# Optimization experiments

Measured on AMD Instinct MI355X. Metric: run time of the kernel, lower is better.

The kernel has to match this reference:

```python
import jax, jax.numpy as jnp
import numpy as np

N_HEADS = 4
ATT_DIM = 640  # 10 * n_channels
SCALE = ATT_DIM ** (-0.5)


def setup_inputs() -> dict:
    key = jax.random.key(0)
    k1, k2, k3, k4, k5 = jax.random.split(key, 5)
    C, HpA = 64, N_HEADS * ATT_DIM  # 64, 2560
    x = jax.random.normal(k1, (8, C, 32, 32), dtype=jnp.float32)
    W_proj = jax.random.normal(k2, (C, 3 * HpA), dtype=jnp.float32) * (C ** -0.5)
    b_proj = jax.random.normal(k3, (3 * HpA,), dtype=jnp.float32) * 0.02
    W_out = jax.random.normal(k4, (HpA, C), dtype=jnp.float32) * (HpA ** -0.5)
    b_out = jax.random.normal(k5, (C,), dtype=jnp.float32) * 0.02
    return {"x": x, "t": 0, "W_proj": W_proj, "b_proj": b_proj, "W_out": W_out, "b_out": b_out}


def reference(x, t, W_proj, b_proj, W_out, b_out):
    del t  # unused, matches original signature
    b, c, w, h = x.shape
    seq = w * h
    xs = x.reshape(b, c, seq).transpose(0, 2, 1)  # [b, seq, C]
    proj = (xs @ W_proj + b_proj).reshape(b, seq, N_HEADS, 3 * ATT_DIM)
    q, k, v = jnp.split(proj, 3, axis=-1)  # each [b, seq, H, D]
    # scores [b, i, j, h]; NOTE softmax over axis=1 (queries), non-standard
    prod = jnp.einsum('bihd,bjhd->bijh', q, k) * SCALE
    soft = jax.nn.softmax(prod, axis=1)
    att = jnp.einsum('bijh,bjhd->bihd', soft, v)  # [b, seq, H, D]
    out = att.reshape(b, seq, N_HEADS * ATT_DIM) @ W_out + b_out  # [b, seq, C]
    out = out + xs
    return out.reshape(b, w, h, c).transpose(0, 3, 1, 2)
```

## Files before the change

kernel.cpp:

```cpp
#include <hip/hip_runtime.h>
#include <hip/hip_bf16.h>
#include <stdint.h>

typedef unsigned short u16;
typedef __attribute__((ext_vector_type(4))) float f32x4;
typedef __attribute__((ext_vector_type(8))) short bf16x8;

#define DEV __device__ __forceinline__

DEV float bf2f(u16 b){ unsigned u = ((unsigned)b) << 16; return __builtin_bit_cast(float, u); }
DEV u16 f2bf(float f){
  unsigned u = __builtin_bit_cast(unsigned, f);
  u += 0x7FFFu + ((u >> 16) & 1u);
  return (u16)(u >> 16);
}

DEV int xcd_swz(int nwg){
  const int bid = (int)blockIdx.x;
  return (bid & 7) * (nwg >> 3) + (bid >> 3);
}

DEV void stage_x64(const u16* srcbase, u16* dst, int tid){
  #pragma unroll
  for (int q = 0; q < 4; q++) {
    const int boff = q * 4096 + tid * 16;
    const int row = boff >> 7, slot = (boff & 127) >> 4;
    const int kk = (slot ^ (row & 7)) << 3;
    __builtin_amdgcn_global_load_lds(
        (const __attribute__((address_space(1))) void*)(srcbase + (long)row * 64 + kk),
        (__attribute__((address_space(3))) void*)(dst + (boff >> 1)), 16, 0, 0);
  }
}

DEV void tr_tile(float (*tile)[65], const float* src, u16* dst,
                 int R, int C, int r0, int c0)
{
  const int t = threadIdx.x;
  const int rr = t >> 2, cc = (t & 3) * 16;
  const float* sp = src + (long)(r0 + rr) * C + (c0 + cc);
  #pragma unroll
  for (int q = 0; q < 16; q++) tile[rr][cc + q] = sp[q];
  __syncthreads();
  u16* dp = dst + (long)(c0 + rr) * R + (r0 + cc);
  #pragma unroll
  for (int q = 0; q < 16; q++) dp[q] = f2bf(tile[cc + q][rr]);
}

__global__ __launch_bounds__(256) void k_misc(
    const float* __restrict__ x, const float* __restrict__ Wp,
    const float* __restrict__ Wo, const float* __restrict__ bp,
    u16* __restrict__ xt, u16* __restrict__ Wot, u16* __restrict__ Wpb,
    u16* __restrict__ xb, float* __restrict__ uh)
{
  __shared__ float tile[64][65];
  const int q = blockIdx.x;
  if (q < 240) {
    const long i = (long)q * 256 + threadIdx.x;
    const f32x4 a = *(const f32x4*)(Wp + i * 8);
    const f32x4 b = *(const f32x4*)(Wp + i * 8 + 4);
    bf16x8 r;
    #pragma unroll
    for (int e = 0; e < 4; e++){ r[e] = (short)f2bf(a[e]); r[e+4] = (short)f2bf(b[e]); }
    *(bf16x8*)(Wpb + i * 8) = r;
  } else if (q < 368) {
    const int p = q - 240, c0 = (p & 15) * 64, b = p >> 4;
    tr_tile(tile, x + (long)b * 65536, xt + (long)b * 65536, 64, 1024, 0, c0);
  } else if (q < 408) {
    const int p = q - 368;
    tr_tile(tile, Wo, Wot, 2560, 64, p * 64, 0);
  } else if (q < 472) {
    const int p = q - 408;
    const int wv = threadIdx.x >> 6, lane = threadIdx.x & 63;
    const int idx = p * 4 + wv;
    const int h = idx >> 6, c = idx & 63;
    const int qb = h * 1920, kb = qb + 640;
    const float* wrow = Wp + (long)c * 7680 + qb;
    float s = 0.f;
    #pragma unroll
    for (int d0 = 0; d0 < 640; d0 += 64)
      s += wrow[d0 + lane] * bp[kb + d0 + lane];
    #pragma unroll
    for (int off = 32; off; off >>= 1) s += __shfl_down(s, off);
    if (lane == 0) uh[idx] = s;
  } else {
    const int ch = (q - 472) * 256 + threadIdx.x;
    const int b = ch / 10240, rem = ch % 10240;
    const int row = rem >> 7, j8 = rem & 127;
    bf16x8 r;
    if (row < 64) {
      const float* sp = x + ((long)b * 64 + row) * 1024 + j8 * 8;
      const f32x4 a = *(const f32x4*)sp;
      const f32x4 bb = *(const f32x4*)(sp + 4);
      #pragma unroll
      for (int e = 0; e < 4; e++){ r[e] = (short)f2bf(a[e]); r[e+4] = (short)f2bf(bb[e]); }
    } else if (row == 64) {
      #pragma unroll
      for (int e = 0; e < 8; e++) r[e] = (short)0x3F80;
    } else {
      #pragma unroll
      for (int e = 0; e < 8; e++) r[e] = 0;
    }
    *(bf16x8*)(xb + ((long)b * 80 + row) * 1024 + j8 * 8) = r;
  }
}

__global__ __launch_bounds__(256) void k_nh(
    const u16* __restrict__ Wot, const float* __restrict__ bp,
    u16* __restrict__ MxT)
{
  const int wv = threadIdx.x >> 6, lane = threadIdx.x & 63;
  const int idx = blockIdx.x * 4 + wv;
  const int h = idx >> 6, cp = idx & 63;
  const u16* wr_ = Wot + (long)cp * 2560 + h * 640;
  const float* bv = bp + h * 1920 + 1280;
  float s = 0.f;
  #pragma unroll
  for (int d0 = 0; d0 < 640; d0 += 64)
    s += bf2f(wr_[d0 + lane]) * bv[d0 + lane];
  #pragma unroll
  for (int off = 32; off; off >>= 1) s += __shfl_down(s, off);
  if (lane == 0) MxT[cp * 320 + h * 80 + 64] = f2bf(s);
  if (lane >= 1 && lane < 16) MxT[cp * 320 + h * 80 + 64 + lane] = 0;
}

template<int BM, int BN, int BK, int WR, int WC, int MF, int NF>
DEV void gemm_nt(const u16* __restrict__ A, const u16* __restrict__ B,
                 int K, long lda, long ldb, int arow0, int brow0,
                 f32x4 (&acc)[MF][NF], u16* As, u16* Bs)
{
  const int tid  = threadIdx.x;
  const int lane = tid & 63;
  const int w    = tid >> 6;
  const int wr   = w / WC, wc = w % WC;
  constexpr int NT   = WR * WC * 64;
  constexpr int AISS = (BM * BK * 2) / (NT * 16);
  constexpr int BISS = (BN * BK * 2) / (NT * 16);
  constexpr int ABUF = BM * BK;
  constexpr int BBUF = BN * BK;

  #pragma unroll
  for (int m = 0; m < MF; m++)
    #pragma unroll
    for (int n = 0; n < NF; n++) acc[m][n] = f32x4{0.f, 0.f, 0.f, 0.f};

  const int frow = lane & 15;
  const int fs   = lane >> 4;

  auto stage = [&](int buf, int kt) {
    #pragma unroll
    for (int q = 0; q < AISS; q++) {
      const int boff = q * NT * 16 + tid * 16;
      const int row  = boff / (BK * 2);
      const int slot = (boff % (BK * 2)) >> 4;
      const int kk   = ((slot ^ (row & 7)) << 3);
      const u16* src = A + (long)(arow0 + row) * lda + kt + kk;
      __builtin_amdgcn_global_load_lds(
          (const __attribute__((address_space(1))) void*)src,
          (__attribute__((address_space(3))) void*)(As + buf * ABUF + (boff >> 1)), 16, 0, 0);
    }
    #pragma unroll
    for (int q = 0; q < BISS; q++) {
      const int boff = q * NT * 16 + tid * 16;
      const int row  = boff / (BK * 2);
      const int slot = (boff % (BK * 2)) >> 4;
      const int kk   = ((slot ^ (row & 7)) << 3);
      const u16* src = B + (long)(brow0 + row) * ldb + kt + kk;
      __builtin_amdgcn_global_load_lds(
          (const __attribute__((address_space(1))) void*)src,
          (__attribute__((address_space(3))) void*)(Bs + buf * BBUF + (boff >> 1)), 16, 0, 0);
    }
  };

  auto compute = [&](int buf) {
    __builtin_amdgcn_s_setprio(1);
    #pragma unroll
    for (int ks = 0; ks < BK / 32; ++ks) {
      bf16x8 af[MF], bfr[NF];
      #pragma unroll
      for (int m = 0; m < MF; m++) {
        const int row  = wr * (MF * 16) + m * 16 + frow;
        const int slot = (ks * 4 + fs) ^ (row & 7);
        af[m] = *(const bf16x8*)(As + buf * ABUF + row * BK + slot * 8);
      }
      #pragma unroll
      for (int n = 0; n < NF; n++) {
        const int row  = wc * (NF * 16) + n * 16 + frow;
        const int slot = (ks * 4 + fs) ^ (row & 7);
        bfr[n] = *(const bf16x8*)(Bs + buf * BBUF + row * BK + slot * 8);
      }
      #pragma unroll
      for (int m = 0; m < MF; m++)
        #pragma unroll
        for (int n = 0; n < NF; n++)
          acc[m][n] = __builtin_amdgcn_mfma_f32_16x16x32_bf16(af[m], bfr[n], acc[m][n], 0, 0, 0);
    }
    __builtin_amdgcn_s_setprio(0);
  };

  stage(0, 0);
  asm volatile("s_waitcnt vmcnt(0)" ::: "memory");
  __syncthreads();
  int cur = 0;
  for (int kt = BK; kt < K; kt += BK) {
    stage(cur ^ 1, kt);
    compute(cur);
    asm volatile("s_waitcnt vmcnt(0)" ::: "memory");
    __syncthreads();
    cur ^= 1;
  }
  compute(cur);
}

template<int MF, int NF, typename FV, typename FS>
DEV void epi_u16(u16* SH, FV&& fval, FS&& fstore)
{
  constexpr int RC = MF * 16, CC = NF * 16, CPR = NF * 2;
  const int lane = threadIdx.x & 63;
  const int w = threadIdx.x >> 6;
  u16* et = SH + w * (RC * CC);
  __syncthreads();
  #pragma unroll
  for (int m = 0; m < MF; m++)
    #pragma unroll
    for (int n = 0; n < NF; n++)
      #pragma unroll
      for (int j = 0; j < 4; j++) {
        const int row = m * 16 + (lane >> 4) * 4 + j;
        const int col = n * 16 + (lane & 15);
        et[row * CC + (((col >> 3) ^ row) & (CPR - 1)) * 8 + (col & 7)] =
            f2bf(fval(m, n, j, row, col));
      }
  constexpr int RPI = 64 / CPR;
  #pragma unroll
  for (int it = 0; it < RC / RPI; ++it) {
    const int row = it * RPI + lane / CPR;
    const int ch  = lane % CPR;
    bf16x8 v = *(const bf16x8*)(et + row * CC + ((ch ^ row) & (CPR - 1)) * 8);
    fstore(row, ch * 8, v);
  }
}

__global__ __launch_bounds__(256) void k_prep(
    const u16* __restrict__ Wpb, const u16* __restrict__ Wot,
    u16* __restrict__ Ahat, u16* __restrict__ MxT)
{
  __shared__ __align__(16) u16 SH[4 * 64 * 64];
  u16* As = SH; u16* Bs = SH + 2 * 64 * 64;
  const int q = blockIdx.x;
  const int w = threadIdx.x >> 6;
  const int wr = w >> 1, wc = w & 1;
  f32x4 acc[2][2];
  if (q < 4) {
    const int h = q;
    gemm_nt<64, 64, 64, 2, 2, 2, 2>(Wpb + h * 1920 + 640, Wpb + h * 1920, 640,
                                    7680, 7680, 0, 0, acc, As, Bs);
    u16* dst = Ahat + h * 4096;
    epi_u16<2, 2>(SH,
      [&](int m, int n, int j, int row, int col){ return acc[m][n][j]; },
      [&](int row, int c0, bf16x8 v){
        *(bf16x8*)(dst + (wr * 32 + row) * 64 + wc * 32 + c0) = v; });
  } else {
    const int h = q - 4;
    gemm_nt<64, 64, 64, 2, 2, 2, 2>(Wot + h * 640, Wpb + h * 1920 + 1280, 640,
                                    2560, 7680, 0, 0, acc, As, Bs);
    epi_u16<2, 2>(SH,
      [&](int m, int n, int j, int row, int col){ return acc[m][n][j]; },
      [&](int row, int c0, bf16x8 v){
        *(bf16x8*)(MxT + (long)(wr * 32 + row) * 320 + h * 80 + wc * 32 + c0) = v; });
  }
}

__global__ __launch_bounds__(256) void k_qkz(
    const u16* __restrict__ xt, const u16* __restrict__ Ahat,
    const float* __restrict__ uh, float* __restrict__ Z)
{
  __shared__ __align__(16) u16 XI[2][8192];
  __shared__ __align__(16) u16 AH[4096];
  __shared__ __align__(16) u16 XJ[8192];
  __shared__ __align__(16) u16 TT[8192];
  __shared__ float uts[128];
  __shared__ float uhl[64];
  __shared__ float Zs[2][128];
  const int tid = threadIdx.x, lane = tid & 63, w = tid >> 6;
  const int frow = lane & 15, fs = lane >> 4;
  const int wr = w >> 1, wc = w & 1;
  const int id = xcd_swz(256);
  const int bh = id >> 3, tj = id & 7;
  const int b = bh >> 2, h = bh & 3;
  const int j0 = b * 1024 + tj * 128;

  #pragma unroll
  for (int q = 0; q < 2; q++) {
    const int boff = q * 4096 + tid * 16;
    const int row = boff >> 7, slot = (boff & 127) >> 4;
    const int kk = (slot ^ (row & 7)) << 3;
    __builtin_amdgcn_global_load_lds(
        (const __attribute__((address_space(1))) void*)(Ahat + h * 4096 + row * 64 + kk),
        (__attribute__((address_space(3))) void*)(AH + (boff >> 1)), 16, 0, 0);
  }
  stage_x64(xt + (long)j0 * 64, XJ, tid);
  stage_x64(xt + (long)(b * 1024) * 64, XI[0], tid);
  if (tid < 64) uhl[tid] = uh[h * 64 + tid];
  asm volatile("s_waitcnt vmcnt(0)" ::: "memory");
  __syncthreads();

  float csum[4] = {0.f, 0.f, 0.f, 0.f};
  int cur = 0;
  for (int it = 0; it < 8; ++it) {
    if (it < 7) stage_x64(xt + (long)(b * 1024 + (it + 1) * 128) * 64, XI[cur ^ 1], tid);
    f32x4 acc1[4][2];
    #pragma unroll
    for (int m = 0; m < 4; m++)
      #pragma unroll
      for (int n = 0; n < 2; n++) acc1[m][n] = f32x4{0.f, 0.f, 0.f, 0.f};
    #pragma unroll
    for (int ks = 0; ks < 2; ks++) {
      bf16x8 af[4], bfr[2];
      #pragma unroll
      for (int m = 0; m < 4; m++) {
        const int row = wr * 64 + m * 16 + frow;
        af[m] = *(const bf16x8*)(XI[cur] + row * 64 + (((ks * 4 + fs) ^ (row & 7)) << 3));
      }
      #pragma unroll
      for (int n = 0; n < 2; n++) {
        const int row = wc * 32 + n * 16 + frow;
        bfr[n] = *(const bf16x8*)(AH + row * 64 + (((ks * 4 + fs) ^ (row & 7)) << 3));
      }
      #pragma unroll
      for (int m = 0; m < 4; m++)
        #pragma unroll
        for (int n = 0; n < 2; n++)
          acc1[m][n] = __builtin_amdgcn_mfma_f32_16x16x32_bf16(af[m], bfr[n], acc1[m][n], 0, 0, 0);
    }
    float su = 0.f;
    if (tid < 128) {
      #pragma unroll
      for (int s = 0; s < 8; s++) {
        bf16x8 v = *(const bf16x8*)(XI[cur] + tid * 64 + ((s ^ (tid & 7)) << 3));
        #pragma unroll
        for (int e = 0; e < 8; e++) su += bf2f((u16)v[e]) * uhl[s * 8 + e];
      }
    }
    __syncthreads();
    if (tid < 128) uts[tid] = su;
    #pragma unroll
    for (int m = 0; m < 4; m++)
      #pragma unroll
      for (int n = 0; n < 2; n++)
        #pragma unroll
        for (int j = 0; j < 4; j++) {
          const int row = wr * 64 + m * 16 + (lane >> 4) * 4 + j;
          const int col = wc * 32 + n * 16 + (lane & 15);
          TT[row * 64 + (((col >> 3) ^ (row & 7)) << 3) + (col & 7)] = f2bf(acc1[m][n][j]);
        }
    asm volatile("s_waitcnt vmcnt(0)" ::: "memory");
    __syncthreads();
    f32x4 sacc[4][4];
    #pragma unroll
    for (int m = 0; m < 4; m++)
      #pragma unroll
      for (int n = 0; n < 4; n++) sacc[m][n] = f32x4{0.f, 0.f, 0.f, 0.f};
    #pragma unroll
    for (int ks = 0; ks < 2; ks++) {
      bf16x8 af[4], bfr[4];
      #pragma unroll
      for (int m = 0; m < 4; m++) {
        const int row = wr * 64 + m * 16 + frow;
        af[m] = *(const bf16x8*)(TT + row * 64 + (((ks * 4 + fs) ^ (row & 7)) << 3));
      }
      #pragma unroll
      for (int n = 0; n < 4; n++) {
        const int row = wc * 64 + n * 16 + frow;
        bfr[n] = *(const bf16x8*)(XJ + row * 64 + (((ks * 4 + fs) ^ (row & 7)) << 3));
      }
      #pragma unroll
      for (int m = 0; m < 4; m++)
        #pragma unroll
        for (int n = 0; n < 4; n++)
          sacc[m][n] = __builtin_amdgcn_mfma_f32_16x16x32_bf16(af[m], bfr[n], sacc[m][n], 0, 0, 0);
    }
    #pragma unroll
    for (int m = 0; m < 4; m++)
      #pragma unroll
      for (int j = 0; j < 4; j++) {
        const float rv = uts[wr * 64 + m * 16 + (lane >> 4) * 4 + j];
        #pragma unroll
        for (int n = 0; n < 4; n++)
          csum[n] += __expf((sacc[m][n][j] + rv) * 0.03952847075210474f);
      }
    cur ^= 1;
  }
  #pragma unroll
  for (int n = 0; n < 4; n++) {
    csum[n] += __shfl_xor(csum[n], 16);
    csum[n] += __shfl_xor(csum[n], 32);
  }
  if ((lane >> 4) == 0) {
    #pragma unroll
    for (int n = 0; n < 4; n++) Zs[wr][wc * 64 + n * 16 + lane] = csum[n];
  }
  __syncthreads();
  if (tid < 128) Z[(long)bh * 1024 + tj * 128 + tid] = Zs[0][tid] + Zs[1][tid];
}

__global__ __launch_bounds__(256) void k_G(
    const u16* __restrict__ xt, const u16* __restrict__ xb,
    const u16* __restrict__ Ahat, const float* __restrict__ uh,
    const float* __restrict__ Z, u16* __restrict__ G)
{
  __shared__ __align__(16) u16 XIT[8192];
  __shared__ __align__(16) u16 AH[4096];
  __shared__ __align__(16) u16 XJ[2][8192];
  __shared__ __align__(16) u16 XB[10240];
  __shared__ __align__(16) u16 PT[16384];
  __shared__ float uts[128];
  __shared__ float uhl[64];
  __shared__ float rzs[128];
  const int tid = threadIdx.x, lane = tid & 63, w = tid >> 6;
  const int frow = lane & 15, fs = lane >> 4;
  const int wr = w >> 1, wc = w & 1;
  const int id = xcd_swz(256);
  const int bh = id >> 3, ti = id & 7;
  const int b = bh >> 2, h = bh & 3;
  const int i0 = b * 1024 + ti * 128;

  #pragma unroll
  for (int q = 0; q < 2; q++) {
    const int boff = q * 4096 + tid * 16;
    const int row = boff >> 7, slot = (boff & 127) >> 4;
    const int kk = (slot ^ (row & 7)) << 3;
    __builtin_amdgcn_global_load_lds(
        (const __attribute__((address_space(1))) void*)(Ahat + h * 4096 + row * 64 + kk),
        (__attribute__((address_space(3))) void*)(AH + (boff >> 1)), 16, 0, 0);
  }
  stage_x64(xt + (long)i0 * 64, XIT, tid);
  stage_x64(xt + (long)(b * 1024) * 64, XJ[0], tid);
  if (tid < 64) uhl[tid] = uh[h * 64 + tid];
  asm volatile("s_waitcnt vmcnt(0)" ::: "memory");
  __syncthreads();

  f32x4 acc1[4][2];
  #pragma unroll
  for (int m = 0; m < 4; m++)
    #pragma unroll
    for (int n = 0; n < 2; n++) acc1[m][n] = f32x4{0.f, 0.f, 0.f, 0.f};
  #pragma unroll
  for (int ks = 0; ks < 2; ks++) {
    bf16x8 af[4], bfr[2];
    #pragma unroll
    for (int m = 0; m < 4; m++) {
      const int row = wr * 64 + m * 16 + frow;
      af[m] = *(const bf16x8*)(XIT + row * 64 + (((ks * 4 + fs) ^ (row & 7)) << 3));
    }
    #pragma unroll
    for (int n = 0; n < 2; n++) {
      const int row = wc * 32 + n * 16 + frow;
      bfr[n] = *(const bf16x8*)(AH + row * 64 + (((ks * 4 + fs) ^ (row & 7)) << 3));
    }
    #pragma unroll
    for (int m = 0; m < 4; m++)
      #pragma unroll
      for (int n = 0; n < 2; n++)
        acc1[m][n] = __builtin_amdgcn_mfma_f32_16x16x32_bf16(af[m], bfr[n], acc1[m][n], 0, 0, 0);
  }
  float su = 0.f;
  if (tid < 128) {
    #pragma unroll
    for (int s = 0; s < 8; s++) {
      bf16x8 v = *(const bf16x8*)(XIT + tid * 64 + ((s ^ (tid & 7)) << 3));
      #pragma unroll
      for (int e = 0; e < 8; e++) su += bf2f((u16)v[e]) * uhl[s * 8 + e];
    }
  }
  __syncthreads();
  if (tid < 128) uts[tid] = su;
  #pragma unroll
  for (int m = 0; m < 4; m++)
    #pragma unroll
    for (int n = 0; n < 2; n++)
      #pragma unroll
      for (int j = 0; j < 4; j++) {
        const int row = wr * 64 + m * 16 + (lane >> 4) * 4 + j;
        const int col = wc * 32 + n * 16 + (lane & 15);
        XIT[row * 64 + (((col >> 3) ^ (row & 7)) << 3) + (col & 7)] = f2bf(acc1[m][n][j]);
      }
  __syncthreads();

  f32x4 gacc[2][5];
  #pragma unroll
  for (int m = 0; m < 2; m++)
    #pragma unroll
    for (int n = 0; n < 5; n++) gacc[m][n] = f32x4{0.f, 0.f, 0.f, 0.f};
  int cur = 0;
  for (int j = 0; j < 8; ++j) {
    #pragma unroll
    for (int q = 0; q < 5; q++) {
      const int boff = q * 4096 + tid * 16;
      const int c = boff >> 8, sl = (boff & 255) >> 4;
      const int kk = (sl ^ (c & 7)) << 3;
      __builtin_amdgcn_global_load_lds(
          (const __attribute__((address_space(1))) void*)(xb + ((long)b * 80 + c) * 1024 + j * 128 + kk),
          (__attribute__((address_space(3))) void*)(XB + (boff >> 1)), 16, 0, 0);
    }
    if (j < 7) stage_x64(xt + (long)(b * 1024 + (j + 1) * 128) * 64, XJ[cur ^ 1], tid);
    if (tid < 128) rzs[tid] = 1.0f / Z[(long)bh * 1024 + j * 128 + tid];
    f32x4 sacc[4][4];
    #pragma unroll
    for (int m = 0; m < 4; m++)
      #pragma unroll
      for (int n = 0; n < 4; n++) sacc[m][n] = f32x4{0.f, 0.f, 0.f, 0.f};
    #pragma unroll
    for (int ks = 0; ks < 2; ks++) {
      bf16x8 af[4], bfr[4];
      #pragma unroll
      for (int m = 0; m < 4; m++) {
        const int row = wr * 64 + m * 16 + frow;
        af[m] = *(const bf16x8*)(XIT + row * 64 + (((ks * 4 + fs) ^ (row & 7)) << 3));
      }
      #pragma unroll
      for (int n = 0; n < 4; n++) {
        const int row = wc * 64 + n * 16 + frow;
        bfr[n] = *(const bf16x8*)(XJ[cur] + row * 64 + (((ks * 4 + fs) ^ (row & 7)) << 3));
      }
      #pragma unroll
      for (int m = 0; m < 4; m++)
        #pragma unroll
        for (int n = 0; n < 4; n++)
          sacc[m][n] = __builtin_amdgcn_mfma_f32_16x16x32_bf16(af[m], bfr[n], sacc[m][n], 0, 0, 0);
    }
    __syncthreads();
    #pragma unroll
    for (int m = 0; m < 4; m++)
      #pragma unroll
      for (int jj = 0; jj < 4; jj++) {
        const int row = wr * 64 + m * 16 + (lane >> 4) * 4 + jj;
        const float rv = uts[row];
        #pragma unroll
        for (int n = 0; n < 4; n++) {
          const int col = wc * 64 + n * 16 + (lane & 15);
          const float p = __expf((sacc[m][n][jj] + rv) * 0.03952847075210474f) * rzs[col];
          PT[row * 128 + (((col >> 3) ^ (row & 7)) << 3) + (col & 7)] = f2bf(p);
        }
      }
    asm volatile("s_waitcnt vmcnt(0)" ::: "memory");
    __syncthreads();
    #pragma unroll
    for (int ks = 0; ks < 4; ks++) {
      bf16x8 af2[2], bfr2[5];
      #pragma unroll
      for (int m = 0; m < 2; m++) {
        const int row = w * 32 + m * 16 + frow;
        af2[m] = *(const bf16x8*)(PT + row * 128 + (((ks * 4 + fs) ^ (row & 7)) << 3));
      }
      #pragma unroll
      for (int n = 0; n < 5; n++) {
        const int rc = n * 16 + frow;
        bfr2[n] = *(const bf16x8*)(XB + rc * 128 + (((ks * 4 + fs) ^ (rc & 7)) << 3));
      }
      #pragma unroll
      for (int m = 0; m < 2; m++)
        #pragma unroll
        for (int n = 0; n < 5; n++)
          gacc[m][n] = __builtin_amdgcn_mfma_f32_16x16x32_bf16(af2[m], bfr2[n], gacc[m][n], 0, 0, 0);
    }
    __syncthreads();
    cur ^= 1;
  }
  #pragma unroll
  for (int m = 0; m < 2; m++)
    #pragma unroll
    for (int n = 0; n < 5; n++)
      #pragma unroll
      for (int jj = 0; jj < 4; jj++) {
        const int row = w * 32 + m * 16 + (lane >> 4) * 4 + jj;
        const int col = n * 16 + (lane & 15);
        PT[row * 80 + col] = f2bf(gacc[m][n][jj]);
      }
  __syncthreads();
  #pragma unroll
  for (int it = 0; it < 5; ++it) {
    const int task = it * 256 + tid;
    const int row = task / 10, ch = task % 10;
    bf16x8 v = *(const bf16x8*)(PT + row * 80 + ch * 8);
    *(bf16x8*)(G + (long)(i0 + row) * 320 + h * 80 + ch * 8) = v;
  }
}

__global__ __launch_bounds__(256) void k_out(
    const u16* __restrict__ G, const u16* __restrict__ MxT,
    const float* __restrict__ bo, const float* __restrict__ x, float* __restrict__ out)
{
  __shared__ __align__(16) u16 SH[2 * 128 * 64 + 2 * 64 * 64];
  u16* As = SH; u16* Bs = SH + 2 * 128 * 64;
  f32x4 acc[2][4];
  gemm_nt<128, 64, 64, 4, 1, 2, 4>(G, MxT, 320, 320, 320,
                                   blockIdx.x * 128, 0, acc, As, Bs);
  const int lane = threadIdx.x & 63;
  const int wr = threadIdx.x >> 6;
  float* etf = (float*)SH;
  __syncthreads();
  #pragma unroll
  for (int m = 0; m < 2; m++)
    #pragma unroll
    for (int n = 0; n < 4; n++)
      #pragma unroll
      for (int j = 0; j < 4; j++) {
        const int sl = wr * 32 + m * 16 + (lane >> 4) * 4 + j;
        const int c  = n * 16 + (lane & 15);
        etf[c * 132 + sl] = acc[m][n][j];
      }
  __syncthreads();
  const int b = blockIdx.x >> 3, s0 = (blockIdx.x & 7) * 128;
  #pragma unroll
  for (int it = 0; it < 8; ++it) {
    const int task = it * 256 + threadIdx.x;
    const int c = task >> 5, q = (task & 31) * 4;
    const float bias = bo[c];
    f32x4 v = *(const f32x4*)(etf + c * 132 + q);
    const long xi = ((long)(b * 64 + c) << 10) + s0 + q;
    const f32x4 xv = *(const f32x4*)(x + xi);
    #pragma unroll
    for (int e = 0; e < 4; e++) v[e] += bias + xv[e];
    *(f32x4*)(out + xi) = v;
  }
}

extern "C" void kernel_launch(void* const* d_in, const int* in_sizes, int n_in,
                              void* d_out, int out_size, void* d_ws, size_t ws_size,
                              hipStream_t stream)
{
  (void)in_sizes; (void)n_in; (void)out_size; (void)ws_size;
  const float* x  = (const float*)d_in[0];
  const float* Wp = (const float*)d_in[2];
  const float* bp = (const float*)d_in[3];
  const float* Wo = (const float*)d_in[4];
  const float* bo = (const float*)d_in[5];
  float* out = (float*)d_out;

  char* w8 = (char*)d_ws;
  u16*   xt   = (u16*)(w8 + 0L);
  u16*   xb   = (u16*)(w8 + 1048576L);
  u16*   Wot  = (u16*)(w8 + 2359296L);
  u16*   Wpb  = (u16*)(w8 + 2686976L);
  u16*   Ahat = (u16*)(w8 + 3670016L);
  u16*   MxT  = (u16*)(w8 + 3702784L);
  float* uh   = (float*)(w8 + 3743744L);
  float* Z    = (float*)(w8 + 3744768L);
  u16*   G    = (u16*)(w8 + 3875840L);

  k_misc<<<792, 256, 0, stream>>>(x, Wp, Wo, bp, xt, Wot, Wpb, xb, uh);
  k_nh  <<<64,  256, 0, stream>>>(Wot, bp, MxT);
  k_prep<<<8,   256, 0, stream>>>(Wpb, Wot, Ahat, MxT);
  k_qkz <<<256, 256, 0, stream>>>(xt, Ahat, uh, Z);
  k_G   <<<256, 256, 0, stream>>>(xt, xb, Ahat, uh, Z, G);
  k_out <<<64,  256, 0, stream>>>(G, MxT, bo, x, out);
}
```

Baseline: 76.74 us.

## Split Z reduction across i-halves, widen k_G to 512 threads, fold k_nh into k_misc

k_qkz now launches 512 blocks, each covering half of the query tiles and writing a partial column sum. k_G sums the two partials when it computes the reciprocal. k_G moves to 512 threads (8 waves) with smaller per-wave tiles, which raises wave-level parallelism per CU and lowers register pressure. The separate k_nh launch is folded into an extra k_misc block that reads fp32 Wo directly, removing one kernel launch, though that single block does serial 640-step loops.

```diff
diff --git a/kernel.cpp b/kernel.cpp
--- a/kernel.cpp
+++ b/kernel.cpp
@@ -20,15 +20,20 @@
   return (bid & 7) * (nwg >> 3) + (bid >> 3);
 }
 
+DEV void gld16(const u16* src, u16* dst){
+  __builtin_amdgcn_global_load_lds(
+      (const __attribute__((address_space(1))) void*)src,
+      (__attribute__((address_space(3))) void*)dst, 16, 0, 0);
+}
+
+template<int NTH>
 DEV void stage_x64(const u16* srcbase, u16* dst, int tid){
   #pragma unroll
-  for (int q = 0; q < 4; q++) {
-    const int boff = q * 4096 + tid * 16;
+  for (int q = 0; q < 16384 / (NTH * 16); q++) {
+    const int boff = q * NTH * 16 + tid * 16;
     const int row = boff >> 7, slot = (boff & 127) >> 4;
     const int kk = (slot ^ (row & 7)) << 3;
-    __builtin_amdgcn_global_load_lds(
-        (const __attribute__((address_space(1))) void*)(srcbase + (long)row * 64 + kk),
-        (__attribute__((address_space(3))) void*)(dst + (boff >> 1)), 16, 0, 0);
+    gld16(srcbase + (long)row * 64 + kk, dst + (boff >> 1));
   }
 }
 
@@ -50,7 +55,7 @@
     const float* __restrict__ x, const float* __restrict__ Wp,
     const float* __restrict__ Wo, const float* __restrict__ bp,
     u16* __restrict__ xt, u16* __restrict__ Wot, u16* __restrict__ Wpb,
-    u16* __restrict__ xb, float* __restrict__ uh)
+    u16* __restrict__ xb, float* __restrict__ uh, u16* __restrict__ MxT)
 {
   __shared__ float tile[64][65];
   const int q = blockIdx.x;
@@ -82,7 +87,7 @@
     #pragma unroll
     for (int off = 32; off; off >>= 1) s += __shfl_down(s, off);
     if (lane == 0) uh[idx] = s;
-  } else {
+  } else if (q < 792) {
     const int ch = (q - 472) * 256 + threadIdx.x;
     const int b = ch / 10240, rem = ch % 10240;
     const int row = rem >> 7, j8 = rem & 127;
@@ -101,26 +106,17 @@
       for (int e = 0; e < 8; e++) r[e] = 0;
     }
     *(bf16x8*)(xb + ((long)b * 80 + row) * 1024 + j8 * 8) = r;
-  }
-}
-
-__global__ __launch_bounds__(256) void k_nh(
-    const u16* __restrict__ Wot, const float* __restrict__ bp,
-    u16* __restrict__ MxT)
-{
-  const int wv = threadIdx.x >> 6, lane = threadIdx.x & 63;
-  const int idx = blockIdx.x * 4 + wv;
-  const int h = idx >> 6, cp = idx & 63;
-  const u16* wr_ = Wot + (long)cp * 2560 + h * 640;
-  const float* bv = bp + h * 1920 + 1280;
-  float s = 0.f;
-  #pragma unroll
-  for (int d0 = 0; d0 < 640; d0 += 64)
-    s += bf2f(wr_[d0 + lane]) * bv[d0 + lane];
-  #pragma unroll
-  for (int off = 32; off; off >>= 1) s += __shfl_down(s, off);
-  if (lane == 0) MxT[cp * 320 + h * 80 + 64] = f2bf(s);
-  if (lane >= 1 && lane < 16) MxT[cp * 320 + h * 80 + 64 + lane] = 0;
+  } else {
+    const int wv = threadIdx.x >> 6, lane = threadIdx.x & 63;
+    const float* bv = bp + wv * 1920 + 1280;
+    float s = 0.f;
+    #pragma unroll 8
+    for (int d = 0; d < 640; d++)
+      s += Wo[(long)(wv * 640 + d) * 64 + lane] * bv[d];
+    MxT[lane * 320 + wv * 80 + 64] = f2bf(s);
+    #pragma unroll
+    for (int e = 1; e < 16; e++) MxT[lane * 320 + wv * 80 + 64 + e] = 0;
+  }
 }
 
 template<int BM, int BN, int BK, int WR, int WC, int MF, int NF>
@@ -153,10 +149,7 @@
       const int row  = boff / (BK * 2);
       const int slot = (boff % (BK * 2)) >> 4;
       const int kk   = ((slot ^ (row & 7)) << 3);
-      const u16* src = A + (long)(arow0 + row) * lda + kt + kk;
-      __builtin_amdgcn_global_load_lds(
-          (const __attribute__((address_space(1))) void*)src,
-          (__attribute__((address_space(3))) void*)(As + buf * ABUF + (boff >> 1)), 16, 0, 0);
+      gld16(A + (long)(arow0 + row) * lda + kt + kk, As + buf * ABUF + (boff >> 1));
     }
     #pragma unroll
     for (int q = 0; q < BISS; q++) {
@@ -164,10 +157,7 @@
       const int row  = boff / (BK * 2);
       const int slot = (boff % (BK * 2)) >> 4;
       const int kk   = ((slot ^ (row & 7)) << 3);
-      const u16* src = B + (long)(brow0 + row) * ldb + kt + kk;
-      __builtin_amdgcn_global_load_lds(
-          (const __attribute__((address_space(1))) void*)src,
-          (__attribute__((address_space(3))) void*)(Bs + buf * BBUF + (boff >> 1)), 16, 0, 0);
+      gld16(B + (long)(brow0 + row) * ldb + kt + kk, Bs + buf * BBUF + (boff >> 1));
     }
   };
 
@@ -272,7 +262,7 @@
 
 __global__ __launch_bounds__(256) void k_qkz(
     const u16* __restrict__ xt, const u16* __restrict__ Ahat,
-    const float* __restrict__ uh, float* __restrict__ Z)
+    const float* __restrict__ uh, float* __restrict__ Zp)
 {
   __shared__ __align__(16) u16 XI[2][8192];
   __shared__ __align__(16) u16 AH[4096];
@@ -284,30 +274,30 @@
   const int tid = threadIdx.x, lane = tid & 63, w = tid >> 6;
   const int frow = lane & 15, fs = lane >> 4;
   const int wr = w >> 1, wc = w & 1;
-  const int id = xcd_swz(256);
-  const int bh = id >> 3, tj = id & 7;
+  const int id = xcd_swz(512);
+  const int bh = id >> 4, rem = id & 15;
+  const int tj = rem >> 1, ihalf = rem & 1;
   const int b = bh >> 2, h = bh & 3;
   const int j0 = b * 1024 + tj * 128;
+  const int itb = ihalf * 4;
 
   #pragma unroll
   for (int q = 0; q < 2; q++) {
     const int boff = q * 4096 + tid * 16;
     const int row = boff >> 7, slot = (boff & 127) >> 4;
     const int kk = (slot ^ (row & 7)) << 3;
-    __builtin_amdgcn_global_load_lds(
-        (const __attribute__((address_space(1))) void*)(Ahat + h * 4096 + row * 64 + kk),
-        (__attribute__((address_space(3))) void*)(AH + (boff >> 1)), 16, 0, 0);
-  }
-  stage_x64(xt + (long)j0 * 64, XJ, tid);
-  stage_x64(xt + (long)(b * 1024) * 64, XI[0], tid);
+    gld16(Ahat + h * 4096 + row * 64 + kk, AH + (boff >> 1));
+  }
+  stage_x64<256>(xt + (long)j0 * 64, XJ, tid);
+  stage_x64<256>(xt + (long)(b * 1024 + itb * 128) * 64, XI[0], tid);
   if (tid < 64) uhl[tid] = uh[h * 64 + tid];
   asm volatile("s_waitcnt vmcnt(0)" ::: "memory");
   __syncthreads();
 
   float csum[4] = {0.f, 0.f, 0.f, 0.f};
   int cur = 0;
-  for (int it = 0; it < 8; ++it) {
-    if (it < 7) stage_x64(xt + (long)(b * 1024 + (it + 1) * 128) * 64, XI[cur ^ 1], tid);
+  for (int it = 0; it < 4; ++it) {
+    if (it < 3) stage_x64<256>(xt + (long)(b * 1024 + (itb + it + 1) * 128) * 64, XI[cur ^ 1], tid);
     f32x4 acc1[4][2];
     #pragma unroll
     for (int m = 0; m < 4; m++)
@@ -400,13 +390,14 @@
     for (int n = 0; n < 4; n++) Zs[wr][wc * 64 + n * 16 + lane] = csum[n];
   }
   __syncthreads();
-  if (tid < 128) Z[(long)bh * 1024 + tj * 128 + tid] = Zs[0][tid] + Zs[1][tid];
-}
-
-__global__ __launch_bounds__(256) void k_G(
+  if (tid < 128)
+    Zp[(long)(ihalf * 32 + bh) * 1024 + tj * 128 + tid] = Zs[0][tid] + Zs[1][tid];
+}
+
+__global__ __launch_bounds__(512) void k_G(
     const u16* __restrict__ xt, const u16* __restrict__ xb,
     const u16* __restrict__ Ahat, const float* __restrict__ uh,
-    const float* __restrict__ Z, u16* __restrict__ G)
+    const float* __restrict__ Zp, u16* __restrict__ G)
 {
   __shared__ __align__(16) u16 XIT[8192];
   __shared__ __align__(16) u16 AH[4096];
@@ -418,50 +409,40 @@
   __shared__ float rzs[128];
   const int tid = threadIdx.x, lane = tid & 63, w = tid >> 6;
   const int frow = lane & 15, fs = lane >> 4;
-  const int wr = w >> 1, wc = w & 1;
+  const int twr = w >> 2, twc = w & 3;
   const int id = xcd_swz(256);
   const int bh = id >> 3, ti = id & 7;
   const int b = bh >> 2, h = bh & 3;
   const int i0 = b * 1024 + ti * 128;
 
-  #pragma unroll
-  for (int q = 0; q < 2; q++) {
-    const int boff = q * 4096 + tid * 16;
+  {
+    const int boff = tid * 16;
     const int row = boff >> 7, slot = (boff & 127) >> 4;
     const int kk = (slot ^ (row & 7)) << 3;
-    __builtin_amdgcn_global_load_lds(
-        (const __attribute__((address_space(1))) void*)(Ahat + h * 4096 + row * 64 + kk),
-        (__attribute__((address_space(3))) void*)(AH + (boff >> 1)), 16, 0, 0);
-  }
-  stage_x64(xt + (long)i0 * 64, XIT, tid);
-  stage_x64(xt + (long)(b * 1024) * 64, XJ[0], tid);
+    gld16(Ahat + h * 4096 + row * 64 + kk, AH + (boff >> 1));
+  }
+  stage_x64<512>(xt + (long)i0 * 64, XIT, tid);
+  stage_x64<512>(xt + (long)(b * 1024) * 64, XJ[0], tid);
   if (tid < 64) uhl[tid] = uh[h * 64 + tid];
   asm volatile("s_waitcnt vmcnt(0)" ::: "memory");
   __syncthreads();
 
-  f32x4 acc1[4][2];
-  #pragma unroll
-  for (int m = 0; m < 4; m++)
-    #pragma unroll
-    for (int n = 0; n < 2; n++) acc1[m][n] = f32x4{0.f, 0.f, 0.f, 0.f};
+  f32x4 acc1[4];
+  #pragma unroll
+  for (int m = 0; m < 4; m++) acc1[m] = f32x4{0.f, 0.f, 0.f, 0.f};
   #pragma unroll
   for (int ks = 0; ks < 2; ks++) {
-    bf16x8 af[4], bfr[2];
+    bf16x8 af[4], bfr;
     #pragma unroll
     for (int m = 0; m < 4; m++) {
-      const int row = wr * 64 + m * 16 + frow;
+      const int row = twr * 64 + m * 16 + frow;
       af[m] = *(const bf16x8*)(XIT + row * 64 + (((ks * 4 + fs) ^ (row & 7)) << 3));
     }
-    #pragma unroll
-    for (int n = 0; n < 2; n++) {
-      const int row = wc * 32 + n * 16 + frow;
-      bfr[n] = *(const bf16x8*)(AH + row * 64 + (((ks * 4 + fs) ^ (row & 7)) << 3));
-    }
+    const int rowb = twc * 16 + frow;
+    bfr = *(const bf16x8*)(AH + rowb * 64 + (((ks * 4 + fs) ^ (rowb & 7)) << 3));
     #pragma unroll
     for (int m = 0; m < 4; m++)
-      #pragma unroll
-      for (int n = 0; n < 2; n++)
-        acc1[m][n] = __builtin_amdgcn_mfma_f32_16x16x32_bf16(af[m], bfr[n], acc1[m][n], 0, 0, 0);
+      acc1[m] = __builtin_amdgcn_mfma_f32_16x16x32_bf16(af[m], bfr, acc1[m], 0, 0, 0);
   }
   float su = 0.f;
   if (tid < 128) {
@@ -477,55 +458,57 @@
   #pragma unroll
   for (int m = 0; m < 4; m++)
     #pragma unroll
-    for (int n = 0; n < 2; n++)
-      #pragma unroll
-      for (int j = 0; j < 4; j++) {
-        const int row = wr * 64 + m * 16 + (lane >> 4) * 4 + j;
-        const int col = wc * 32 + n * 16 + (lane & 15);
-        XIT[row * 64 + (((col >> 3) ^ (row & 7)) << 3) + (col & 7)] = f2bf(acc1[m][n][j]);
-      }
-  __syncthreads();
-
-  f32x4 gacc[2][5];
-  #pragma unroll
-  for (int m = 0; m < 2; m++)
-    #pragma unroll
-    for (int n = 0; n < 5; n++) gacc[m][n] = f32x4{0.f, 0.f, 0.f, 0.f};
+    for (int j = 0; j < 4; j++) {
+      const int row = twr * 64 + m * 16 + (lane >> 4) * 4 + j;
+      const int col = twc * 16 + (lane & 15);
+      XIT[row * 64 + (((col >> 3) ^ (row & 7)) << 3) + (col & 7)] = f2bf(acc1[m][j]);
+    }
+  __syncthreads();
+
+  f32x4 gacc[5];
+  #pragma unroll
+  for (int n = 0; n < 5; n++) gacc[n] = f32x4{0.f, 0.f, 0.f, 0.f};
   int cur = 0;
   for (int j = 0; j < 8; ++j) {
     #pragma unroll
-    for (int q = 0; q < 5; q++) {
-      const int boff = q * 4096 + tid * 16;
+    for (int q = 0; q < 2; q++) {
+      const int boff = q * 8192 + tid * 16;
       const int c = boff >> 8, sl = (boff & 255) >> 4;
       const int kk = (sl ^ (c & 7)) << 3;
-      __builtin_amdgcn_global_load_lds(
-          (const __attribute__((address_space(1))) void*)(xb + ((long)b * 80 + c) * 1024 + j * 128 + kk),
-          (__attribute__((address_space(3))) void*)(XB + (boff >> 1)), 16, 0, 0);
-    }
-    if (j < 7) stage_x64(xt + (long)(b * 1024 + (j + 1) * 128) * 64, XJ[cur ^ 1], tid);
-    if (tid < 128) rzs[tid] = 1.0f / Z[(long)bh * 1024 + j * 128 + tid];
-    f32x4 sacc[4][4];
+      gld16(xb + ((long)b * 80 + c) * 1024 + j * 128 + kk, XB + (boff >> 1));
+    }
+    if (tid < 256) {
+      const int boff = 16384 + tid * 16;
+      const int c = boff >> 8, sl = (boff & 255) >> 4;
+      const int kk = (sl ^ (c & 7)) << 3;
+      gld16(xb + ((long)b * 80 + c) * 1024 + j * 128 + kk, XB + (boff >> 1));
+    }
+    if (j < 7) stage_x64<512>(xt + (long)(b * 1024 + (j + 1) * 128) * 64, XJ[cur ^ 1], tid);
+    if (tid < 128)
+      rzs[tid] = 1.0f / (Zp[(long)bh * 1024 + j * 128 + tid] +
+                         Zp[(long)(32 + bh) * 1024 + j * 128 + tid]);
+    f32x4 sacc[4][2];
     #pragma unroll
     for (int m = 0; m < 4; m++)
       #pragma unroll
-      for (int n = 0; n < 4; n++) sacc[m][n] = f32x4{0.f, 0.f, 0.f, 0.f};
+      for (int n = 0; n < 2; n++) sacc[m][n] = f32x4{0.f, 0.f, 0.f, 0.f};
     #pragma unroll
     for (int ks = 0; ks < 2; ks++) {
-      bf16x8 af[4], bfr[4];
+      bf16x8 af[4], bfr[2];
       #pragma unroll
       for (int m = 0; m < 4; m++) {
-        const int row = wr * 64 + m * 16 + frow;
+        const int row = twr * 64 + m * 16 + frow;
         af[m] = *(const bf16x8*)(XIT + row * 64 + (((ks * 4 + fs) ^ (row & 7)) << 3));
       }
       #pragma unroll
-      for (int n = 0; n < 4; n++) {
-        const int row = wc * 64 + n * 16 + frow;
+      for (int n = 0; n < 2; n++) {
+        const int row = twc * 32 + n * 16 + frow;
         bfr[n] = *(const bf16x8*)(XJ[cur] + row * 64 + (((ks * 4 + fs) ^ (row & 7)) << 3));
       }
       #pragma unroll
       for (int m = 0; m < 4; m++)
         #pragma unroll
-        for (int n = 0; n < 4; n++)
+        for (int n = 0; n < 2; n++)
           sacc[m][n] = __builtin_amdgcn_mfma_f32_16x16x32_bf16(af[m], bfr[n], sacc[m][n], 0, 0, 0);
     }
     __syncthreads();
@@ -533,11 +516,11 @@
     for (int m = 0; m < 4; m++)
       #pragma unroll
       for (int jj = 0; jj < 4; jj++) {
-        const int row = wr * 64 + m * 16 + (lane >> 4) * 4 + jj;
+        const int row = twr * 64 + m * 16 + (lane >> 4) * 4 + jj;
         const float rv = uts[row];
         #pragma unroll
-        for (int n = 0; n < 4; n++) {
-          const int col = wc * 64 + n * 16 + (lane & 15);
+        for (int n = 0; n < 2; n++) {
+          const int col = twc * 32 + n * 16 + (lane & 15);
           const float p = __expf((sacc[m][n][jj] + rv) * 0.03952847075210474f) * rzs[col];
           PT[row * 128 + (((col >> 3) ^ (row & 7)) << 3) + (col & 7)] = f2bf(p);
         }
@@ -546,40 +529,39 @@
     __syncthreads();
     #pragma unroll
     for (int ks = 0; ks < 4; ks++) {
-      bf16x8 af2[2], bfr2[5];
-      #pragma unroll
-      for (int m = 0; m < 2; m++) {
-        const int row = w * 32 + m * 16 + frow;
-        af2[m] = *(const bf16x8*)(PT + row * 128 + (((ks * 4 + fs) ^ (row & 7)) << 3));
-      }
+      bf16x8 af2, bfr2[5];
+      const int row = w * 16 + frow;
+      af2 = *(const bf16x8*)(PT + row * 128 + (((ks * 4 + fs) ^ (row & 7)) << 3));
       #pragma unroll
       for (int n = 0; n < 5; n++) {
         const int rc = n * 16 + frow;
         bfr2[n] = *(const bf16x8*)(XB + rc * 128 + (((ks * 4 + fs) ^ (rc & 7)) << 3));
       }
       #pragma unroll
-      for (int m = 0; m < 2; m++)
-        #pragma unroll
-        for (int n = 0; n < 5; n++)
-          gacc[m][n] = __builtin_amdgcn_mfma_f32_16x16x32_bf16(af2[m], bfr2[n], gacc[m][n], 0, 0, 0);
+      for (int n = 0; n < 5; n++)
+        gacc[n] = __builtin_amdgcn_mfma_f32_16x16x32_bf16(af2, bfr2[n], gacc[n], 0, 0, 0);
     }
     __syncthreads();
     cur ^= 1;
   }
   #pragma unroll
-  for (int m = 0; m < 2; m++)
-    #pragma unroll
-    for (int n = 0; n < 5; n++)
-      #pragma unroll
-      for (int jj = 0; jj < 4; jj++) {
-        const int row = w * 32 + m * 16 + (lane >> 4) * 4 + jj;
-        const int col = n * 16 + (lane & 15);
-        PT[row * 80 + col] = f2bf(gacc[m][n][jj]);
-      }
-  __syncthreads();
-  #pragma unroll
-  for (int it = 0; it < 5; ++it) {
-    const int task = it * 256 + tid;
+  for (int n = 0; n < 5; n++)
+    #pragma unroll
+    for (int jj = 0; jj < 4; jj++) {
+      const int row = w * 16 + (lane >> 4) * 4 + jj;
+      const int col = n * 16 + (lane & 15);
+      PT[row * 80 + col] = f2bf(gacc[n][jj]);
+    }
+  __syncthreads();
+  #pragma unroll
+  for (int it = 0; it < 2; ++it) {
+    const int task = it * 512 + tid;
+    const int row = task / 10, ch = task % 10;
+    bf16x8 v = *(const bf16x8*)(PT + row * 80 + ch * 8);
+    *(bf16x8*)(G + (long)(i0 + row) * 320 + h * 80 + ch * 8) = v;
+  }
+  if (tid < 256) {
+    const int task = 1024 + tid;
     const int row = task / 10, ch = task % 10;
     bf16x8 v = *(const bf16x8*)(PT + row * 80 + ch * 8);
     *(bf16x8*)(G + (long)(i0 + row) * 320 + h * 80 + ch * 8) = v;
@@ -645,13 +627,12 @@
   u16*   Ahat = (u16*)(w8 + 3670016L);
   u16*   MxT  = (u16*)(w8 + 3702784L);
   float* uh   = (float*)(w8 + 3743744L);
-  float* Z    = (float*)(w8 + 3744768L);
-  u16*   G    = (u16*)(w8 + 3875840L);
-
-  k_misc<<<792, 256, 0, stream>>>(x, Wp, Wo, bp, xt, Wot, Wpb, xb, uh);
-  k_nh  <<<64,  256, 0, stream>>>(Wot, bp, MxT);
+  float* Zp   = (float*)(w8 + 3744768L);
+  u16*   G    = (u16*)(w8 + 4006912L);
+
+  k_misc<<<793, 256, 0, stream>>>(x, Wp, Wo, bp, xt, Wot, Wpb, xb, uh, MxT);
   k_prep<<<8,   256, 0, stream>>>(Wpb, Wot, Ahat, MxT);
-  k_qkz <<<256, 256, 0, stream>>>(xt, Ahat, uh, Z);
-  k_G   <<<256, 256, 0, stream>>>(xt, xb, Ahat, uh, Z, G);
+  k_qkz <<<512, 256, 0, stream>>>(xt, Ahat, uh, Zp);
+  k_G   <<<256, 512, 0, stream>>>(xt, xb, Ahat, uh, Zp, G);
   k_out <<<64,  256, 0, stream>>>(G, MxT, bo, x, out);
 }
```

New measurement: 79.60 us. 1.04x slower.
